# Performance work log

Hardware: AMD Instinct MI355X
Metric: run time of the kernel (lower is better)

Reference implementation:

```python
import jax, jax.numpy as jnp
import numpy as np

NUM_ITERATIONS = 3
B, M, P, D, O, I = 32, 32, 196, 20, 16, 8


def squash(s, axis=-1):
    # v = (||s||^2 / (1+||s||^2)) * s/||s||
    sq = jnp.sum(s * s, axis=axis, keepdims=True)
    return (sq / (1.0 + sq)) * s / jnp.sqrt(sq + 1e-9)


def setup_inputs() -> dict:
    key = jax.random.key(0)
    kx, kw = jax.random.split(key)
    x = jax.random.normal(kx, (B, M, P, I), dtype=jnp.float32)
    W = jax.random.normal(kw, (1, M, P, D, O, I), dtype=jnp.float32)
    return {"x": x, "W": W}


def reference(x, W):
    b_, m, p, i = x.shape
    Wm = W[0]  # [M,P,D,O,I]
    # u_hat = W @ u : batched matvec -> [B,M,P,D,O]
    u_hat = jnp.einsum('mpdoi,bmpi->bmpdo', Wm, x)
    d = u_hat.shape[3]
    b = jnp.zeros((b_, m, p, d), dtype=x.dtype)
    c = None
    v = None
    for it in range(NUM_ITERATIONS):
        # softmax jointly over (num_in_caps * num_digit_cap), matching view+softmax(dim=2)
        c = jax.nn.softmax(b.reshape(b_, m, p * d), axis=2).reshape(b_, m, p, d)
        # s = sum over maps and in-caps of c * u_hat -> [B,D,O]
        s = jnp.einsum('bmpd,bmpdo->bdo', c, u_hat)
        v = squash(s, axis=-1)
        if it != NUM_ITERATIONS - 1:
            # agreement: u_hat^T v -> [B,M,P,D]
            b = b + jnp.einsum('bmpdo,bdo->bmpd', u_hat, v)
    map_size = int(np.sqrt(p))
    weighted = c[..., None] * u_hat  # [B,M,P,D,O]
    xm = weighted.reshape(b_, m, map_size, map_size, d, -1)
    c_maps = jnp.sqrt(jnp.sum(xm * xm, axis=-1))  # [B,M,ms,ms,D]
    features = jnp.mean(weighted, axis=2)  # [B,M,D,O]
    return v, c_maps, features
```

## Files before the change

kernel.cpp:

```cpp
#include <hip/hip_runtime.h>
#include <math.h>

#define B_   32
#define M_   32
#define P_   196
#define D_   20
#define O_   16
#define I_   8
#define DO_  320
#define PD_  3920
#define ROW_ 62720

#define CMAPS_OFF 10240
#define FEAT_OFF  4024320

__device__ __forceinline__ unsigned short f2bf(float v) {
    unsigned int u = __float_as_uint(v);
    return (unsigned short)((u + 0x7fffu + ((u >> 16) & 1u)) >> 16);
}
__device__ __forceinline__ unsigned int pk2(float lo, float hi) {
    return (unsigned int)f2bf(lo) | ((unsigned int)f2bf(hi) << 16);
}
__device__ __forceinline__ float bfhi(unsigned int w) { return __uint_as_float(w & 0xffff0000u); }
__device__ __forceinline__ float bflo(unsigned int w) { return __uint_as_float(w << 16); }

__device__ __forceinline__ void gload16(const float* g, float* l) {
    __builtin_amdgcn_global_load_lds(
        (const __attribute__((address_space(1))) void*)g,
        (__attribute__((address_space(3))) void*)l, 16, 0, 0);
}

#define CPT_ 2
#define CNT_ 98
__global__ __launch_bounds__(320)
void caps_u(const float* __restrict__ x, const float* __restrict__ W,
            unsigned short* __restrict__ uh)
{
    __shared__ float4 wb[2][640];
    __shared__ float  xl[512];

    const int m  = blockIdx.x / CNT_;
    const int pt = blockIdx.x % CNT_;
    const int p0 = pt * CPT_;
    const int t  = threadIdx.x;
    const int g  = t % 40;
    const int bq = t / 40;
    const int wl = t & ~63;

    if (t < 128) {
        int b = t >> 2, q = t & 3;
        *(float4*)(xl + b * 16 + q * 4) =
            *(const float4*)(x + (((size_t)b * M_ + m) * P_ + p0 + (q >> 1)) * I_
                             + (q & 1) * 4);
    }
    {
        const float* ws0 = W + (size_t)(m * P_ + p0) * 2560;
        #pragma unroll
        for (int q = 0; q < 2; q++) {
            int s = q * 320 + t;
            gload16(ws0 + (size_t)(s ^ ((s >> 4) & 7)) * 4,
                    (float*)&wb[0][q * 320 + wl]);
        }
    }
    __syncthreads();

    #pragma unroll
    for (int h = 0; h < 2; h++) {
        if (h == 0) {
            const float* ws1 = W + (size_t)(m * P_ + p0 + 1) * 2560;
            #pragma unroll
            for (int q = 0; q < 2; q++) {
                int s = q * 320 + t;
                gload16(ws1 + (size_t)(s ^ ((s >> 4) & 7)) * 4,
                        (float*)&wb[1][q * 320 + wl]);
            }
        }
        const int pl = h;
        float xr[4][8];
        #pragma unroll
        for (int bb = 0; bb < 4; bb++) {
            *(float4*)(xr[bb])     = *(float4*)(xl + (bq * 4 + bb) * 16 + pl * 8);
            *(float4*)(xr[bb] + 4) = *(float4*)(xl + (bq * 4 + bb) * 16 + pl * 8 + 4);
        }
        const float4* wp = wb[h];
        #pragma unroll
        for (int r = 0; r < 4; r++) {
            const int gb = 4 * g + 160 * r;
            const int hx = (gb >> 4) & 7;
            float4 w0 = wp[(gb + 0) ^ hx];
            float4 w1 = wp[(gb + 1) ^ hx];
            float4 w2 = wp[(gb + 2) ^ hx];
            float4 w3 = wp[(gb + 3) ^ hx];
            const int do0 = 2 * g + 80 * r;
            #pragma unroll
            for (int bb = 0; bb < 4; bb++) {
                const float* a = xr[bb];
                float u0 = w0.x * a[0];
                u0 = fmaf(w0.y, a[1], u0); u0 = fmaf(w0.z, a[2], u0);
                u0 = fmaf(w0.w, a[3], u0); u0 = fmaf(w1.x, a[4], u0);
                u0 = fmaf(w1.y, a[5], u0); u0 = fmaf(w1.z, a[6], u0);
                u0 = fmaf(w1.w, a[7], u0);
                float u1 = w2.x * a[0];
                u1 = fmaf(w2.y, a[1], u1); u1 = fmaf(w2.z, a[2], u1);
                u1 = fmaf(w2.w, a[3], u1); u1 = fmaf(w3.x, a[4], u1);
                u1 = fmaf(w3.y, a[5], u1); u1 = fmaf(w3.z, a[6], u1);
                u1 = fmaf(w3.w, a[7], u1);
                *(unsigned int*)(uh + (((size_t)(bq * 4 + bb) * M_ + m) * P_
                                       + p0 + pl) * DO_ + do0) = pk2(u0, u1);
            }
        }
        if (h == 0) __syncthreads();
    }
}

template<int MODE>
__global__ __launch_bounds__(320)
void route_k(const unsigned short* __restrict__ uh, const float* __restrict__ vin,
             float* __restrict__ pbm, float* __restrict__ out)
{
    extern __shared__ float sm[];
    float* accL  = sm;
    float* red   = sm + 320 * 17;
    float* blogL = red + 16;
    float* usqL  = blogL + 3920;

    const int blk = blockIdx.x;
    const int t = threadIdx.x;
    const int d = t % 20;
    const int k = t / 20;
    const int pstart = k * 12 + (k < 4 ? k : 4);
    const int pcnt   = (k < 4) ? 13 : 12;
    const unsigned short* up = uh + (size_t)blk * ROW_ + d * 16;

    float vreg[16];
    if (MODE) {
        const float* vb = vin + (size_t)(blk >> 5) * DO_;
        #pragma unroll
        for (int o = 0; o < 16; o++) vreg[o] = vb[d * 16 + o];
    }
    float acc[16];
    #pragma unroll
    for (int o = 0; o < 16; o++) acc[o] = 0.f;
    float mloc = -1e30f, Z = 0.f;

    float4 a0 = ((const float4*)(up + (size_t)pstart * DO_))[0];
    float4 a1 = ((const float4*)(up + (size_t)pstart * DO_))[1];

    for (int pp = 0; pp < pcnt; pp++) {
        const int p  = pstart + pp;
        const int pn = pstart + ((pp + 1 < pcnt) ? pp + 1 : pp);
        float4 n0 = ((const float4*)(up + (size_t)pn * DO_))[0];
        float4 n1 = ((const float4*)(up + (size_t)pn * DO_))[1];

        unsigned int ua[8];
        ua[0]=__float_as_uint(a0.x); ua[1]=__float_as_uint(a0.y);
        ua[2]=__float_as_uint(a0.z); ua[3]=__float_as_uint(a0.w);
        ua[4]=__float_as_uint(a1.x); ua[5]=__float_as_uint(a1.y);
        ua[6]=__float_as_uint(a1.z); ua[7]=__float_as_uint(a1.w);
        float u[16];
        #pragma unroll
        for (int q = 0; q < 8; q++) { u[2*q] = bflo(ua[q]); u[2*q+1] = bfhi(ua[q]); }

        if (MODE) {
            float bl = u[0] * vreg[0];
            #pragma unroll
            for (int o = 1; o < 16; o++) bl = fmaf(u[o], vreg[o], bl);
            if (MODE == 2) {
                float us = u[0] * u[0];
                #pragma unroll
                for (int o = 1; o < 16; o++) us = fmaf(u[o], u[o], us);
                blogL[p * D_ + d] = bl;
                usqL[p * D_ + d]  = us;
            }
            if (bl > mloc + 8.f) {
                float r = __expf(mloc - bl);
                Z *= r;
                #pragma unroll
                for (int o = 0; o < 16; o++) acc[o] *= r;
                mloc = bl;
            }
            float e = __expf(bl - mloc);
            Z += e;
            #pragma unroll
            for (int o = 0; o < 16; o++) acc[o] = fmaf(e, u[o], acc[o]);
        } else {
            #pragma unroll
            for (int o = 0; o < 16; o++) acc[o] += u[o];
        }
        a0 = n0; a1 = n1;
    }

    float f = 1.f, iz = 1.f, mx = 0.f;
    if (MODE) {
        mx = mloc;
        #pragma unroll
        for (int msk = 1; msk < 64; msk <<= 1) mx = fmaxf(mx, __shfl_xor(mx, msk, 64));
        if ((t & 63) == 0) red[t >> 6] = mx;
        __syncthreads();
        mx = fmaxf(fmaxf(fmaxf(red[0], red[1]), fmaxf(red[2], red[3])), red[4]);
        f = __expf(mloc - mx);
        float zz = Z * f;
        #pragma unroll
        for (int msk = 1; msk < 64; msk <<= 1) zz += __shfl_xor(zz, msk, 64);
        if ((t & 63) == 0) red[8 + (t >> 6)] = zz;
        __syncthreads();
        iz = 1.f / (red[8] + red[9] + red[10] + red[11] + red[12]);
    }
    #pragma unroll
    for (int o = 0; o < 16; o++) accL[t * 17 + o] = acc[o] * f;
    __syncthreads();
    {
        const int dd = t >> 4, oo = t & 15;
        float s = 0.f;
        #pragma unroll
        for (int kk = 0; kk < 16; kk++) s += accL[(kk * 20 + dd) * 17 + oo];
        s *= iz;
        pbm[(size_t)blk * DO_ + t] = s;
        if (MODE == 2) out[FEAT_OFF + (size_t)blk * DO_ + t] = s * (1.f / 196.f);
    }
    if (MODE == 2) {
        for (int e = t; e < PD_; e += 320)
            out[CMAPS_OFF + (size_t)blk * PD_ + e] =
                __expf(blogL[e] - mx) * iz * sqrtf(usqL[e]);
    }
}

template<int WH>
__global__ __launch_bounds__(320)
void sq2_k(const float* __restrict__ pbm, float* __restrict__ v1,
           float* __restrict__ vs, float* __restrict__ out)
{
    const int b = blockIdx.x, t = threadIdx.x;
    float s = 0.f;
    for (int mi = 0; mi < M_; mi++) s += pbm[((size_t)b * M_ + mi) * DO_ + t];
    if (WH == 0) s *= (1.f / PD_);
    float sq = s * s;
    #pragma unroll
    for (int msk = 1; msk < 16; msk <<= 1) sq += __shfl_xor(sq, msk, 16);
    float vr = (sq / (1.f + sq)) * s * rsqrtf(sq + 1e-9f);
    if (WH == 0) v1[(size_t)b * DO_ + t] = vr;
    if (WH == 1) vs[(size_t)b * DO_ + t] = v1[(size_t)b * DO_ + t] + vr;
    if (WH == 2) out[(size_t)b * DO_ + t] = vr;
}

extern "C" void kernel_launch(void* const* d_in, const int* in_sizes, int n_in,
                              void* d_out, int out_size, void* d_ws, size_t ws_size,
                              hipStream_t stream)
{
    const float* x = (const float*)d_in[0];
    const float* W = (const float*)d_in[1];
    float* out = (float*)d_out;

    unsigned short* uh = (unsigned short*)d_ws;
    float* fws = (float*)((char*)d_ws + (size_t)64225280 * 2);
    float* pbm = fws;
    float* v1  = pbm + (size_t)B_ * M_ * DO_;
    float* vs  = v1 + (size_t)B_ * DO_;

    const size_t LDS_A = (320 * 17 + 16) * sizeof(float);
    const size_t LDS_B = LDS_A + 2 * PD_ * sizeof(float);

    caps_u<<<M_ * CNT_, 320, 0, stream>>>(x, W, uh);

    route_k<0><<<B_ * M_, 320, LDS_A, stream>>>(uh, v1, pbm, out);
    sq2_k<0><<<B_, 320, 0, stream>>>(pbm, v1, vs, out);

    route_k<1><<<B_ * M_, 320, LDS_A, stream>>>(uh, v1, pbm, out);
    sq2_k<1><<<B_, 320, 0, stream>>>(pbm, v1, vs, out);

    route_k<2><<<B_ * M_, 320, LDS_B, stream>>>(uh, vs, pbm, out);
    sq2_k<2><<<B_, 320, 0, stream>>>(pbm, v1, vs, out);
}
```

Measured before the change: 117.1 us.

## Fuse squash reductions into routing kernels and use hardware bf16 packing

```diff
diff --git a/kernel.cpp b/kernel.cpp
--- a/kernel.cpp
+++ b/kernel.cpp
@@ -1,4 +1,5 @@
 #include <hip/hip_runtime.h>
+#include <hip/hip_bf16.h>
 #include <math.h>
 
 #define B_   32
@@ -14,12 +15,10 @@
 #define CMAPS_OFF 10240
 #define FEAT_OFF  4024320
 
-__device__ __forceinline__ unsigned short f2bf(float v) {
-    unsigned int u = __float_as_uint(v);
-    return (unsigned short)((u + 0x7fffu + ((u >> 16) & 1u)) >> 16);
-}
 __device__ __forceinline__ unsigned int pk2(float lo, float hi) {
-    return (unsigned int)f2bf(lo) | ((unsigned int)f2bf(hi) << 16);
+    union { __hip_bfloat162 h; unsigned int u; } cv;
+    cv.h = __float22bfloat162_rn(make_float2(lo, hi));
+    return cv.u;
 }
 __device__ __forceinline__ float bfhi(unsigned int w) { return __uint_as_float(w & 0xffff0000u); }
 __device__ __forceinline__ float bflo(unsigned int w) { return __uint_as_float(w << 16); }
@@ -115,8 +114,9 @@
 
 template<int MODE>
 __global__ __launch_bounds__(320)
-void route_k(const unsigned short* __restrict__ uh, const float* __restrict__ vin,
-             float* __restrict__ pbm, float* __restrict__ out)
+void route_k(const unsigned short* __restrict__ uh, const float* __restrict__ pin,
+             float* __restrict__ v1g, float* __restrict__ pbm,
+             float* __restrict__ out)
 {
     extern __shared__ float sm[];
     float* accL  = sm;
@@ -125,6 +125,8 @@
     float* usqL  = blogL + 3920;
 
     const int blk = blockIdx.x;
+    const int b   = blk >> 5;
+    const int mm  = blk & 31;
     const int t = threadIdx.x;
     const int d = t % 20;
     const int k = t / 20;
@@ -134,9 +136,21 @@
 
     float vreg[16];
     if (MODE) {
-        const float* vb = vin + (size_t)(blk >> 5) * DO_;
-        #pragma unroll
-        for (int o = 0; o < 16; o++) vreg[o] = vb[d * 16 + o];
+        float s = 0.f;
+        #pragma unroll 8
+        for (int mi = 0; mi < M_; mi++) s += pin[((size_t)b * M_ + mi) * DO_ + t];
+        if (MODE == 1) s *= (1.f / PD_);
+        float sq = s * s;
+        #pragma unroll
+        for (int msk = 1; msk < 16; msk <<= 1) sq += __shfl_xor(sq, msk, 16);
+        float vr = (sq / (1.f + sq)) * s * rsqrtf(sq + 1e-9f);
+        if (MODE == 2) vr += v1g[b * DO_ + t];
+        else if (mm == 0) v1g[b * DO_ + t] = vr;
+        accL[t] = vr;
+        __syncthreads();
+        #pragma unroll
+        for (int o = 0; o < 16; o++) vreg[o] = accL[d * 16 + o];
+        __syncthreads();
     }
     float acc[16];
     #pragma unroll
@@ -225,22 +239,18 @@
     }
 }
 
-template<int WH>
 __global__ __launch_bounds__(320)
-void sq2_k(const float* __restrict__ pbm, float* __restrict__ v1,
-           float* __restrict__ vs, float* __restrict__ out)
+void sqf_k(const float* __restrict__ pbm, float* __restrict__ out)
 {
     const int b = blockIdx.x, t = threadIdx.x;
     float s = 0.f;
+    #pragma unroll 8
     for (int mi = 0; mi < M_; mi++) s += pbm[((size_t)b * M_ + mi) * DO_ + t];
-    if (WH == 0) s *= (1.f / PD_);
     float sq = s * s;
     #pragma unroll
     for (int msk = 1; msk < 16; msk <<= 1) sq += __shfl_xor(sq, msk, 16);
     float vr = (sq / (1.f + sq)) * s * rsqrtf(sq + 1e-9f);
-    if (WH == 0) v1[(size_t)b * DO_ + t] = vr;
-    if (WH == 1) vs[(size_t)b * DO_ + t] = v1[(size_t)b * DO_ + t] + vr;
-    if (WH == 2) out[(size_t)b * DO_ + t] = vr;
+    out[(size_t)b * DO_ + t] = vr;
 }
 
 extern "C" void kernel_launch(void* const* d_in, const int* in_sizes, int n_in,
@@ -253,21 +263,17 @@
 
     unsigned short* uh = (unsigned short*)d_ws;
     float* fws = (float*)((char*)d_ws + (size_t)64225280 * 2);
-    float* pbm = fws;
-    float* v1  = pbm + (size_t)B_ * M_ * DO_;
-    float* vs  = v1 + (size_t)B_ * DO_;
+    float* pbmA = fws;
+    float* pbmB = pbmA + (size_t)B_ * M_ * DO_;
+    float* v1g  = pbmB + (size_t)B_ * M_ * DO_;
 
     const size_t LDS_A = (320 * 17 + 16) * sizeof(float);
     const size_t LDS_B = LDS_A + 2 * PD_ * sizeof(float);
 
     caps_u<<<M_ * CNT_, 320, 0, stream>>>(x, W, uh);
 
-    route_k<0><<<B_ * M_, 320, LDS_A, stream>>>(uh, v1, pbm, out);
-    sq2_k<0><<<B_, 320, 0, stream>>>(pbm, v1, vs, out);
-
-    route_k<1><<<B_ * M_, 320, LDS_A, stream>>>(uh, v1, pbm, out);
-    sq2_k<1><<<B_, 320, 0, stream>>>(pbm, v1, vs, out);
-
-    route_k<2><<<B_ * M_, 320, LDS_B, stream>>>(uh, vs, pbm, out);
-    sq2_k<2><<<B_, 320, 0, stream>>>(pbm, v1, vs, out);
-}
+    route_k<0><<<B_ * M_, 320, LDS_A, stream>>>(uh, nullptr, v1g, pbmA, out);
+    route_k<1><<<B_ * M_, 320, LDS_A, stream>>>(uh, pbmA, v1g, pbmB, out);
+    route_k<2><<<B_ * M_, 320, LDS_B, stream>>>(uh, pbmB, v1g, pbmA, out);
+    sqf_k<<<B_, 320, 0, stream>>>(pbmA, out);
+}
```

Result: no change. 115.4 us (median of 2 runs) (-1.4%).
